# Performance work log

Measured on AMD Instinct MI355X. Metric: run time of the kernel, lower is better.

Reference implementation:

```python
import jax, jax.numpy as jnp
import numpy as np

H, HD, D = 16, 64, 1024
SCALE = HD ** -0.5
TEMP = 1.0
EPS = 1e-5

def setup_inputs() -> dict:
    key = jax.random.key(0)
    ks = jax.random.split(key, 10)
    B, N = 2, 2048
    lim = 1.0 / np.sqrt(D)
    def lin(k, out_d, in_d):
        k1, k2 = jax.random.split(k)
        W = jax.random.uniform(k1, (out_d, in_d), jnp.float32, -lim, lim)
        b = jax.random.uniform(k2, (out_d,), jnp.float32, -lim, lim)
        return W, b
    Wq, bq = lin(ks[0], H * HD, D)
    Wk, bk = lin(ks[1], H * HD, D)
    Wv, bv = lin(ks[2], H * HD, D)
    Wo, bo = lin(ks[3], D, H * HD)
    return {
        "x": jax.random.normal(ks[4], (B, N, D), jnp.float32),
        "adaptive_scale": jnp.ones((H,), jnp.float32),
        "Wq": Wq, "bq": bq, "Wk": Wk, "bk": bk, "Wv": Wv, "bv": bv,
        "Wo": Wo, "bo": bo,
        "gamma": jnp.ones((D,), jnp.float32),
        "beta": jnp.zeros((D,), jnp.float32),
    }

def reference(x, adaptive_scale, Wq, bq, Wk, bk, Wv, bv, Wo, bo, gamma, beta):
    B, N, _ = x.shape
    # self-attention: context = x
    Q = (x @ Wq.T + bq).reshape(B, N, H, HD)
    K = (x @ Wk.T + bk).reshape(B, N, H, HD)
    V = (x @ Wv.T + bv).reshape(B, N, H, HD)
    # per-head adaptive scale folded into scores (matches naive QK^T * scale / temp)
    scores = jnp.einsum('bnhd,bmhd->bhnm', Q, K)
    scores = scores * (SCALE * adaptive_scale)[None, :, None, None] / TEMP
    w = jax.nn.softmax(scores, axis=-1)  # [B,H,N,N]
    attn = jnp.einsum('bhnm,bmhd->bnhd', w, V).reshape(B, N, H * HD)
    y = x + (attn @ Wo.T + bo)
    mu = jnp.mean(y, axis=-1, keepdims=True)
    var = jnp.var(y, axis=-1, keepdims=True)
    return (y - mu) / jnp.sqrt(var + EPS) * gamma + beta
```

## Files before the change

kernel.cpp:

```cpp
#include <hip/hip_runtime.h>
#include <hip/hip_bf16.h>

using bf16 = __hip_bfloat16;
typedef __attribute__((ext_vector_type(8))) short short8;
typedef __attribute__((ext_vector_type(4))) float f32x4;

#define MFMA16(a, b, c) __builtin_amdgcn_mfma_f32_16x16x32_bf16((a), (b), (c), 0, 0, 0)

__device__ inline void async16(bf16* lds, const bf16* g) {
  __builtin_amdgcn_global_load_lds(
      (const __attribute__((address_space(1))) void*)g,
      (__attribute__((address_space(3))) void*)lds, 16, 0, 0);
}

__global__ __launch_bounds__(256) void cvt_all(
    const float* __restrict__ x,  const float* __restrict__ Wq,
    const float* __restrict__ Wk, const float* __restrict__ Wv,
    const float* __restrict__ Wo,
    bf16* __restrict__ xb, bf16* __restrict__ Wqb, bf16* __restrict__ Wkb,
    bf16* __restrict__ Wvb, bf16* __restrict__ Wob) {
  int i = blockIdx.x * 256 + threadIdx.x;
  const float* s; bf16* d; int off;
  if (i < 1048576)      { s = x;  d = xb;  off = i; }
  else if (i < 1310720) { s = Wq; d = Wqb; off = i - 1048576; }
  else if (i < 1572864) { s = Wk; d = Wkb; off = i - 1310720; }
  else if (i < 1835008) { s = Wv; d = Wvb; off = i - 1572864; }
  else                  { s = Wo; d = Wob; off = i - 1835008; }
  float4 v = ((const float4*)s)[off];
  struct __align__(8) B4 { bf16 a, b, c, d; };
  B4 o{__float2bfloat16(v.x), __float2bfloat16(v.y),
       __float2bfloat16(v.z), __float2bfloat16(v.w)};
  *(B4*)&d[(size_t)off * 4] = o;
}

__global__ __launch_bounds__(256) void gemm_qkv(
    const bf16* __restrict__ A,
    const bf16* __restrict__ Wq, const bf16* __restrict__ Wk, const bf16* __restrict__ Wv,
    const float* __restrict__ bq, const float* __restrict__ bk, const float* __restrict__ bv,
    const float* __restrict__ asc,
    bf16* __restrict__ Qb, bf16* __restrict__ Kb, bf16* __restrict__ Vtb) {
  __shared__ __align__(16) bf16 As[128 * 32];
  __shared__ __align__(16) bf16 Bs[128 * 32];

  const int tid = threadIdx.x;
  const int lane = tid & 63;
  const int w = tid >> 6;
  const int m0 = blockIdx.x * 128;
  const int region = blockIdx.y >> 3;
  const int n0loc = (blockIdx.y & 7) * 128;
  const int wm = (w >> 1) * 64;
  const int wn = (w & 1) * 64;
  const int rq = lane & 15;
  const int quad = lane >> 4;
  const int kq = quad * 8;

  const bf16* W = region == 0 ? Wq : (region == 1 ? Wk : Wv);
  const float* bias = region == 0 ? bq : (region == 1 ? bk : bv);
  bf16* C = region == 0 ? Qb : (region == 1 ? Kb : Vtb);

  f32x4 acc[4][4] = {};
  const bf16* Ag = A + (size_t)m0 * 1024;
  const bf16* Wg = W + (size_t)n0loc * 1024;

  for (int k0 = 0; k0 < 1024; k0 += 32) {
    __syncthreads();
#pragma unroll
    for (int rep = 0; rep < 2; ++rep) {
      int c = tid + rep * 256;
      int row = c >> 2;
      int ce = (c & 3) * 8;
      async16(&As[c * 8], Ag + (size_t)row * 1024 + k0 + ce);
      async16(&Bs[c * 8], Wg + (size_t)row * 1024 + k0 + ce);
    }
    __syncthreads();

    short8 a[4], b[4];
#pragma unroll
    for (int i = 0; i < 4; ++i) a[i] = *(const short8*)&As[(wm + i * 16 + rq) * 32 + kq];
#pragma unroll
    for (int j = 0; j < 4; ++j) b[j] = *(const short8*)&Bs[(wn + j * 16 + rq) * 32 + kq];
#pragma unroll
    for (int i = 0; i < 4; ++i)
#pragma unroll
      for (int j = 0; j < 4; ++j) acc[i][j] = MFMA16(a[i], b[j], acc[i][j]);
  }

  const float LOG2E = 1.44269504088896f;
#pragma unroll
  for (int i = 0; i < 4; ++i)
#pragma unroll
    for (int j = 0; j < 4; ++j)
#pragma unroll
      for (int r2 = 0; r2 < 4; ++r2) {
        int m = m0 + wm + i * 16 + quad * 4 + r2;
        int nr = n0loc + wn + j * 16 + rq;
        int bb = m >> 11, t = m & 2047, h = nr >> 6, hd = nr & 63;
        float v = acc[i][j][r2] + bias[nr];
        if (region == 0) v *= 0.125f * asc[h] * LOG2E;
        bf16 ov = __float2bfloat16(v);
        if (region < 2)
          C[(((size_t)(bb * 16 + h)) * 2048 + t) * 64 + hd] = ov;
        else
          C[(((size_t)(bb * 16 + h)) * 64 + hd) * 2048 + t] = ov;
      }
}

__global__ __launch_bounds__(256) void gemm_out(
    const bf16* __restrict__ A, const bf16* __restrict__ W,
    const float* __restrict__ bias, const float* __restrict__ R,
    float* __restrict__ Y) {
  __shared__ __align__(16) bf16 As[128 * 32];
  __shared__ __align__(16) bf16 Bs[128 * 32];

  const int tid = threadIdx.x;
  const int lane = tid & 63;
  const int w = tid >> 6;
  const int m0 = blockIdx.x * 128;
  const int n0 = blockIdx.y * 128;
  const int wm = (w >> 1) * 64;
  const int wn = (w & 1) * 64;
  const int rq = lane & 15;
  const int quad = lane >> 4;
  const int kq = quad * 8;

  f32x4 acc[4][4] = {};
  const bf16* Ag = A + (size_t)m0 * 1024;
  const bf16* Wg = W + (size_t)n0 * 1024;

  for (int k0 = 0; k0 < 1024; k0 += 32) {
    __syncthreads();
#pragma unroll
    for (int rep = 0; rep < 2; ++rep) {
      int c = tid + rep * 256;
      int row = c >> 2;
      int ce = (c & 3) * 8;
      async16(&As[c * 8], Ag + (size_t)row * 1024 + k0 + ce);
      async16(&Bs[c * 8], Wg + (size_t)row * 1024 + k0 + ce);
    }
    __syncthreads();

    short8 a[4], b[4];
#pragma unroll
    for (int i = 0; i < 4; ++i) a[i] = *(const short8*)&As[(wm + i * 16 + rq) * 32 + kq];
#pragma unroll
    for (int j = 0; j < 4; ++j) b[j] = *(const short8*)&Bs[(wn + j * 16 + rq) * 32 + kq];
#pragma unroll
    for (int i = 0; i < 4; ++i)
#pragma unroll
      for (int j = 0; j < 4; ++j) acc[i][j] = MFMA16(a[i], b[j], acc[i][j]);
  }

#pragma unroll
  for (int i = 0; i < 4; ++i)
#pragma unroll
    for (int j = 0; j < 4; ++j)
#pragma unroll
      for (int r2 = 0; r2 < 4; ++r2) {
        int m = m0 + wm + i * 16 + quad * 4 + r2;
        int n = n0 + wn + j * 16 + rq;
        Y[(size_t)m * 1024 + n] = acc[i][j][r2] + bias[n] + R[(size_t)m * 1024 + n];
      }
}

#define LP 72
__global__ __launch_bounds__(256, 3) void attn_kernel(
    const bf16* __restrict__ Qb, const bf16* __restrict__ Kb,
    const bf16* __restrict__ Vtb, bf16* __restrict__ Ob) {
  __shared__ __align__(16) bf16 Ks[64 * 64];
  __shared__ __align__(16) bf16 Vs[64 * 64];
  __shared__ __align__(16) bf16 Ps[4][32 * LP];

  const int q0 = blockIdx.x * 128;
  const int h = blockIdx.y;
  const int b = blockIdx.z;
  const int tid = threadIdx.x;
  const int lane = tid & 63;
  const int w = tid >> 6;
  const int rq = lane & 15;
  const int quad = lane >> 4;
  const int kq = quad * 8;

  const size_t head = ((size_t)(b * 16 + h)) * 2048 * 64;
  const bf16* Qh = Qb + head;
  const bf16* Kh = Kb + head;
  const bf16* Vh = Vtb + head;

  short8 aq[2][2];
#pragma unroll
  for (int s = 0; s < 2; ++s) {
    const bf16* qrow = Qh + (size_t)(q0 + w * 32 + s * 16 + rq) * 64;
    aq[s][0] = *(const short8*)&qrow[kq];
    aq[s][1] = *(const short8*)&qrow[kq + 32];
  }

  short8 ones;
#pragma unroll
  for (int i = 0; i < 8; ++i) ones[i] = (short)0x3F80;

  const int srow = lane >> 3;
  const int sws = ((lane & 7) ^ srow) * 8;
  const int c0 = (quad ^ (rq & 7)) * 8;
  const int c1 = c0 ^ 32;

  f32x4 accO[2][4] = {};
  f32x4 lacc[2] = {};

  for (int kt = 0; kt < 32; ++kt) {
    __syncthreads();
#pragma unroll
    for (int t = 0; t < 2; ++t) {
      int rb = w * 16 + t * 8;
      int row = rb + srow;
      async16(&Ks[rb * 64 + lane * 8], Kh + (size_t)(kt * 64 + row) * 64 + sws);
      async16(&Vs[rb * 64 + lane * 8], Vh + (size_t)row * 2048 + kt * 64 + sws);
    }
    __syncthreads();

    f32x4 S[2][4] = {};
#pragma unroll
    for (int j = 0; j < 4; ++j) {
      short8 bk0 = *(const short8*)&Ks[(j * 16 + rq) * 64 + c0];
      short8 bk1 = *(const short8*)&Ks[(j * 16 + rq) * 64 + c1];
      S[0][j] = MFMA16(aq[0][0], bk0, S[0][j]);
      S[0][j] = MFMA16(aq[0][1], bk1, S[0][j]);
      S[1][j] = MFMA16(aq[1][0], bk0, S[1][j]);
      S[1][j] = MFMA16(aq[1][1], bk1, S[1][j]);
    }

#pragma unroll
    for (int s = 0; s < 2; ++s)
#pragma unroll
      for (int r = 0; r < 4; ++r)
#pragma unroll
        for (int j = 0; j < 4; ++j)
          Ps[w][(s * 16 + quad * 4 + r) * LP + j * 16 + rq] =
              __float2bfloat16(exp2f(S[s][j][r]));

    short8 ap[2][2];
#pragma unroll
    for (int s = 0; s < 2; ++s) {
      ap[s][0] = *(const short8*)&Ps[w][(s * 16 + rq) * LP + kq];
      ap[s][1] = *(const short8*)&Ps[w][(s * 16 + rq) * LP + kq + 32];
    }

#pragma unroll
    for (int dt = 0; dt < 4; ++dt) {
      short8 bv0 = *(const short8*)&Vs[(dt * 16 + rq) * 64 + c0];
      short8 bv1 = *(const short8*)&Vs[(dt * 16 + rq) * 64 + c1];
#pragma unroll
      for (int s = 0; s < 2; ++s) {
        accO[s][dt] = MFMA16(ap[s][0], bv0, accO[s][dt]);
        accO[s][dt] = MFMA16(ap[s][1], bv1, accO[s][dt]);
      }
    }
#pragma unroll
    for (int s = 0; s < 2; ++s) {
      lacc[s] = MFMA16(ap[s][0], ones, lacc[s]);
      lacc[s] = MFMA16(ap[s][1], ones, lacc[s]);
    }
  }

#pragma unroll
  for (int s = 0; s < 2; ++s) {
    float rl[4];
#pragma unroll
    for (int r = 0; r < 4; ++r) rl[r] = 1.f / lacc[s][r];
#pragma unroll
    for (int dt = 0; dt < 4; ++dt)
#pragma unroll
      for (int r = 0; r < 4; ++r) {
        int t = q0 + w * 32 + s * 16 + quad * 4 + r;
        int d = dt * 16 + rq;
        Ob[((size_t)(b * 2048 + t)) * 1024 + h * 64 + d] =
            __float2bfloat16(accO[s][dt][r] * rl[r]);
      }
  }
}

__global__ __launch_bounds__(256) void ln_kernel(
    const float* __restrict__ Y, const float* __restrict__ gamma,
    const float* __restrict__ beta, float* __restrict__ out) {
  const int row = blockIdx.x;
  const int tid = threadIdx.x;
  const int lane = tid & 63;
  const int w = tid >> 6;
  const float* y = Y + (size_t)row * 1024;

  float4 v = *(const float4*)&y[tid * 4];
  float s = v.x + v.y + v.z + v.w;
  float ss = v.x * v.x + v.y * v.y + v.z * v.z + v.w * v.w;
#pragma unroll
  for (int msk = 1; msk < 64; msk <<= 1) {
    s += __shfl_xor(s, msk);
    ss += __shfl_xor(ss, msk);
  }
  __shared__ float red[2][4];
  if (lane == 0) { red[0][w] = s; red[1][w] = ss; }
  __syncthreads();
  s = red[0][0] + red[0][1] + red[0][2] + red[0][3];
  ss = red[1][0] + red[1][1] + red[1][2] + red[1][3];
  float mean = s * (1.f / 1024.f);
  float var = ss * (1.f / 1024.f) - mean * mean;
  float rstd = rsqrtf(var + 1e-5f);
  float4 g = *(const float4*)&gamma[tid * 4];
  float4 bt = *(const float4*)&beta[tid * 4];
  float4 o;
  o.x = (v.x - mean) * rstd * g.x + bt.x;
  o.y = (v.y - mean) * rstd * g.y + bt.y;
  o.z = (v.z - mean) * rstd * g.z + bt.z;
  o.w = (v.w - mean) * rstd * g.w + bt.w;
  *(float4*)&out[(size_t)row * 1024 + tid * 4] = o;
}

extern "C" void kernel_launch(void* const* d_in, const int* in_sizes, int n_in,
                              void* d_out, int out_size, void* d_ws, size_t ws_size,
                              hipStream_t stream) {
  const float* x     = (const float*)d_in[0];
  const float* asc   = (const float*)d_in[1];
  const float* Wq    = (const float*)d_in[2];
  const float* bq    = (const float*)d_in[3];
  const float* Wk    = (const float*)d_in[4];
  const float* bk    = (const float*)d_in[5];
  const float* Wv    = (const float*)d_in[6];
  const float* bv    = (const float*)d_in[7];
  const float* Wo    = (const float*)d_in[8];
  const float* bo    = (const float*)d_in[9];
  const float* gamma = (const float*)d_in[10];
  const float* beta  = (const float*)d_in[11];
  float* out = (float*)d_out;

  char* ws = (char*)d_ws;
  const size_t MB = 1024 * 1024;
  bf16* Qb   = (bf16*)(ws);
  bf16* Kb   = (bf16*)(ws + 8 * MB);
  bf16* Vtb  = (bf16*)(ws + 16 * MB);
  bf16* attn = (bf16*)(ws + 24 * MB);
  bf16* xb   = (bf16*)(ws + 32 * MB);
  bf16* Wqb  = (bf16*)(ws + 40 * MB);
  bf16* Wkb  = (bf16*)(ws + 42 * MB);
  bf16* Wvb  = (bf16*)(ws + 44 * MB);
  bf16* Wob  = (bf16*)(ws + 46 * MB);
  float* y   = (float*)(ws);

  dim3 bb(256);

  cvt_all<<<dim3(8192), bb, 0, stream>>>(x, Wq, Wk, Wv, Wo, xb, Wqb, Wkb, Wvb, Wob);
  gemm_qkv<<<dim3(32, 24), bb, 0, stream>>>(xb, Wqb, Wkb, Wvb, bq, bk, bv, asc, Qb, Kb, Vtb);
  attn_kernel<<<dim3(16, 16, 2), bb, 0, stream>>>(Qb, Kb, Vtb, attn);
  gemm_out<<<dim3(32, 8), bb, 0, stream>>>(attn, Wob, bo, x, y);
  ln_kernel<<<dim3(4096), bb, 0, stream>>>(y, gamma, beta, out);
}
```

Measured before the change: 235.8 us.

## Double-buffer K/V tiles in attention to overlap loads with compute

Splits the shared K and V tiles into two buffers and prefetches the next key tile with async global-to-LDS loads while the current tile is used for QK^T, softmax and PV. One of the two barriers per iteration goes away, and global load latency can overlap with MFMA work. LDS use per block grows by 16 KB, which may limit occupancy. The compiler may also insert conservative memory waits before the LDS reads, which would remove the overlap.

```diff
diff --git a/kernel.cpp b/kernel.cpp
--- a/kernel.cpp
+++ b/kernel.cpp
@@ -166,8 +166,8 @@
 __global__ __launch_bounds__(256, 3) void attn_kernel(
     const bf16* __restrict__ Qb, const bf16* __restrict__ Kb,
     const bf16* __restrict__ Vtb, bf16* __restrict__ Ob) {
-  __shared__ __align__(16) bf16 Ks[64 * 64];
-  __shared__ __align__(16) bf16 Vs[64 * 64];
+  __shared__ __align__(16) bf16 Ks[2][64 * 64];
+  __shared__ __align__(16) bf16 Vs[2][64 * 64];
   __shared__ __align__(16) bf16 Ps[4][32 * LP];
 
   const int q0 = blockIdx.x * 128;
@@ -202,25 +202,35 @@
   const int c0 = (quad ^ (rq & 7)) * 8;
   const int c1 = c0 ^ 32;
 
+  const int rb0 = w * 16;
+  const int rb1 = w * 16 + 8;
+
   f32x4 accO[2][4] = {};
   f32x4 lacc[2] = {};
 
+  {
+    async16(&Ks[0][rb0 * 64 + lane * 8], Kh + (size_t)(rb0 + srow) * 64 + sws);
+    async16(&Vs[0][rb0 * 64 + lane * 8], Vh + (size_t)(rb0 + srow) * 2048 + sws);
+    async16(&Ks[0][rb1 * 64 + lane * 8], Kh + (size_t)(rb1 + srow) * 64 + sws);
+    async16(&Vs[0][rb1 * 64 + lane * 8], Vh + (size_t)(rb1 + srow) * 2048 + sws);
+  }
+
   for (int kt = 0; kt < 32; ++kt) {
-    __syncthreads();
-#pragma unroll
-    for (int t = 0; t < 2; ++t) {
-      int rb = w * 16 + t * 8;
-      int row = rb + srow;
-      async16(&Ks[rb * 64 + lane * 8], Kh + (size_t)(kt * 64 + row) * 64 + sws);
-      async16(&Vs[rb * 64 + lane * 8], Vh + (size_t)row * 2048 + kt * 64 + sws);
-    }
-    __syncthreads();
+    const int cur = kt & 1, nxt = cur ^ 1;
+    __syncthreads();
+    if (kt + 1 < 32) {
+      int g = (kt + 1) * 64;
+      async16(&Ks[nxt][rb0 * 64 + lane * 8], Kh + (size_t)(g + rb0 + srow) * 64 + sws);
+      async16(&Vs[nxt][rb0 * 64 + lane * 8], Vh + (size_t)(rb0 + srow) * 2048 + g + sws);
+      async16(&Ks[nxt][rb1 * 64 + lane * 8], Kh + (size_t)(g + rb1 + srow) * 64 + sws);
+      async16(&Vs[nxt][rb1 * 64 + lane * 8], Vh + (size_t)(rb1 + srow) * 2048 + g + sws);
+    }
 
     f32x4 S[2][4] = {};
 #pragma unroll
     for (int j = 0; j < 4; ++j) {
-      short8 bk0 = *(const short8*)&Ks[(j * 16 + rq) * 64 + c0];
-      short8 bk1 = *(const short8*)&Ks[(j * 16 + rq) * 64 + c1];
+      short8 bk0 = *(const short8*)&Ks[cur][(j * 16 + rq) * 64 + c0];
+      short8 bk1 = *(const short8*)&Ks[cur][(j * 16 + rq) * 64 + c1];
       S[0][j] = MFMA16(aq[0][0], bk0, S[0][j]);
       S[0][j] = MFMA16(aq[0][1], bk1, S[0][j]);
       S[1][j] = MFMA16(aq[1][0], bk0, S[1][j]);
@@ -245,8 +255,8 @@
 
 #pragma unroll
     for (int dt = 0; dt < 4; ++dt) {
-      short8 bv0 = *(const short8*)&Vs[(dt * 16 + rq) * 64 + c0];
-      short8 bv1 = *(const short8*)&Vs[(dt * 16 + rq) * 64 + c1];
+      short8 bv0 = *(const short8*)&Vs[cur][(dt * 16 + rq) * 64 + c0];
+      short8 bv1 = *(const short8*)&Vs[cur][(dt * 16 + rq) * 64 + c1];
 #pragma unroll
       for (int s = 0; s < 2; ++s) {
         accO[s][dt] = MFMA16(ap[s][0], bv0, accO[s][dt]);
```

After: 241.4 us. +2.4%, slower.

## Split attention over two key halves and merge partials in a combine kernel

Applied to the files above, without the earlier changes.

The attention kernel now splits the key sequence into two halves along the grid z dimension, doubling the block count. Each half writes unnormalized bf16 partial outputs and per-row softmax denominators into reused workspace buffers. A new combine kernel sums the two partials and divides by the summed denominators. The aim is better GPU occupancy, since the previous grid underfilled the CUs. The cost is an extra launch, extra global traffic for the partials, and extra bf16 rounding of the unnormalized partials.

```diff
diff --git a/kernel.cpp b/kernel.cpp
--- a/kernel.cpp
+++ b/kernel.cpp
@@ -165,14 +165,16 @@
 #define LP 72
 __global__ __launch_bounds__(256, 3) void attn_kernel(
     const bf16* __restrict__ Qb, const bf16* __restrict__ Kb,
-    const bf16* __restrict__ Vtb, bf16* __restrict__ Ob) {
+    const bf16* __restrict__ Vtb,
+    bf16* __restrict__ P0, bf16* __restrict__ P1, float* __restrict__ lbuf) {
   __shared__ __align__(16) bf16 Ks[64 * 64];
   __shared__ __align__(16) bf16 Vs[64 * 64];
   __shared__ __align__(16) bf16 Ps[4][32 * LP];
 
   const int q0 = blockIdx.x * 128;
   const int h = blockIdx.y;
-  const int b = blockIdx.z;
+  const int b = blockIdx.z & 1;
+  const int half = blockIdx.z >> 1;
   const int tid = threadIdx.x;
   const int lane = tid & 63;
   const int w = tid >> 6;
@@ -205,7 +207,8 @@
   f32x4 accO[2][4] = {};
   f32x4 lacc[2] = {};
 
-  for (int kt = 0; kt < 32; ++kt) {
+  const int kt0 = half * 16;
+  for (int kt = kt0; kt < kt0 + 16; ++kt) {
     __syncthreads();
 #pragma unroll
     for (int t = 0; t < 2; ++t) {
@@ -260,21 +263,49 @@
     }
   }
 
+  bf16* Pout = half ? P1 : P0;
+  float* lout = lbuf + half * 65536;
 #pragma unroll
   for (int s = 0; s < 2; ++s) {
-    float rl[4];
-#pragma unroll
-    for (int r = 0; r < 4; ++r) rl[r] = 1.f / lacc[s][r];
 #pragma unroll
     for (int dt = 0; dt < 4; ++dt)
 #pragma unroll
       for (int r = 0; r < 4; ++r) {
         int t = q0 + w * 32 + s * 16 + quad * 4 + r;
         int d = dt * 16 + rq;
-        Ob[((size_t)(b * 2048 + t)) * 1024 + h * 64 + d] =
-            __float2bfloat16(accO[s][dt][r] * rl[r]);
-      }
-  }
+        Pout[((size_t)(b * 2048 + t)) * 1024 + h * 64 + d] =
+            __float2bfloat16(accO[s][dt][r]);
+      }
+    if (rq == 0) {
+#pragma unroll
+      for (int r = 0; r < 4; ++r) {
+        int t = q0 + w * 32 + s * 16 + quad * 4 + r;
+        lout[(b * 16 + h) * 2048 + t] = lacc[s][r];
+      }
+    }
+  }
+}
+
+__global__ __launch_bounds__(256) void combine_kernel(
+    bf16* __restrict__ P0, const bf16* __restrict__ P1,
+    const float* __restrict__ lbuf) {
+  const int row = blockIdx.x;
+  const int tid = threadIdx.x;
+  const int col = tid * 4;
+  const int b = row >> 11, t = row & 2047;
+  const int h = col >> 6;
+  const float l = lbuf[(b * 16 + h) * 2048 + t] + lbuf[65536 + (b * 16 + h) * 2048 + t];
+  const float rl = 1.f / l;
+  size_t base = (size_t)row * 1024 + col;
+  struct __align__(8) B4 { bf16 a, b, c, d; };
+  B4 p0 = *(const B4*)&P0[base];
+  B4 p1 = *(const B4*)&P1[base];
+  B4 o;
+  o.a = __float2bfloat16((__bfloat162float(p0.a) + __bfloat162float(p1.a)) * rl);
+  o.b = __float2bfloat16((__bfloat162float(p0.b) + __bfloat162float(p1.b)) * rl);
+  o.c = __float2bfloat16((__bfloat162float(p0.c) + __bfloat162float(p1.c)) * rl);
+  o.d = __float2bfloat16((__bfloat162float(p0.d) + __bfloat162float(p1.d)) * rl);
+  *(B4*)&P0[base] = o;
 }
 
 __global__ __launch_bounds__(256) void ln_kernel(
@@ -341,12 +372,15 @@
   bf16* Wvb  = (bf16*)(ws + 44 * MB);
   bf16* Wob  = (bf16*)(ws + 46 * MB);
   float* y   = (float*)(ws);
+  bf16* P1   = xb;
+  float* lbuf = (float*)Wqb;
 
   dim3 bb(256);
 
   cvt_all<<<dim3(8192), bb, 0, stream>>>(x, Wq, Wk, Wv, Wo, xb, Wqb, Wkb, Wvb, Wob);
   gemm_qkv<<<dim3(32, 24), bb, 0, stream>>>(xb, Wqb, Wkb, Wvb, bq, bk, bv, asc, Qb, Kb, Vtb);
-  attn_kernel<<<dim3(16, 16, 2), bb, 0, stream>>>(Qb, Kb, Vtb, attn);
+  attn_kernel<<<dim3(16, 16, 4), bb, 0, stream>>>(Qb, Kb, Vtb, attn, P1, lbuf);
+  combine_kernel<<<dim3(4096), bb, 0, stream>>>(attn, P1, lbuf);
   gemm_out<<<dim3(32, 8), bb, 0, stream>>>(attn, Wob, bo, x, y);
   ln_kernel<<<dim3(4096), bb, 0, stream>>>(y, gamma, beta, out);
 }
```

Measured after the change: 240.6 us. 2.1% more time.
